# Performance work log

Measured on AMD Instinct MI355X. Metric: run time of the kernel, lower is better.

Reference implementation:

```python
import jax, jax.numpy as jnp
import numpy as np

B = 1024   # env batch (rollout step, T=1)
F = 512    # feature_size ('big' conv tower)
H = 128    # LSTM hidden size


def _conv(x, W, b, stride):
    # x: [B,Cin,H,W], W: [Cout,Cin,kh,kw]  (PyTorch NCHW / OIHW, VALID padding)
    y = jax.lax.conv_general_dilated(x, W, (stride, stride), 'VALID',
                                     dimension_numbers=('NCHW', 'OIHW', 'NCHW'))
    return y + b[None, :, None, None]


def _tower(x, W1, b1, W2, b2, W3, b3, Wl, bl):
    y = jax.nn.relu(_conv(x, W1, b1, 4))   # [B,32,20,20]
    y = jax.nn.relu(_conv(y, W2, b2, 2))   # [B,64,9,9]
    y = jax.nn.relu(_conv(y, W3, b3, 1))   # [B,64,7,7]
    y = y.reshape(y.shape[0], -1)          # [B,3136]
    return jax.nn.relu(y @ Wl.T + bl)      # [B,512]


def _ln(x, g, b):
    m = jnp.mean(x, -1, keepdims=True)
    v = jnp.var(x, -1, keepdims=True)
    return (x - m) * jax.lax.rsqrt(v + 1e-5) * g + b


def setup_inputs() -> dict:
    key = jax.random.key(0)
    ks = iter(jax.random.split(key, 64))
    rn = lambda shape, s=0.05: jax.random.normal(next(ks), shape, jnp.float32) * s
    inp = {
        'x': jax.random.normal(next(ks), (B, 2, 84, 84), jnp.float32),
        'done': (jax.random.uniform(next(ks), (B,)) < 0.1).astype(jnp.float32),
        'h0': rn((1, B, H), 0.1),
        'c0': rn((1, B, H), 0.1),
        # video tower
        'vW1': rn((32, 1, 8, 8)), 'vb1': jnp.zeros((32,), jnp.float32),
        'vW2': rn((64, 32, 4, 4)), 'vb2': jnp.zeros((64,), jnp.float32),
        'vW3': rn((64, 64, 3, 3)), 'vb3': jnp.zeros((64,), jnp.float32),
        'vWl': rn((F, 64 * 7 * 7)), 'vbl': jnp.zeros((F,), jnp.float32),
        # audio tower
        'aW1': rn((32, 1, 8, 8)), 'ab1': jnp.zeros((32,), jnp.float32),
        'aW2': rn((64, 32, 4, 4)), 'ab2': jnp.zeros((64,), jnp.float32),
        'aW3': rn((64, 64, 3, 3)), 'ab3': jnp.zeros((64,), jnp.float32),
        'aWl': rn((F, 64 * 7 * 7)), 'abl': jnp.zeros((F,), jnp.float32),
        # LayerNorms
        'vln_g': jnp.ones((F,), jnp.float32), 'vln_b': jnp.zeros((F,), jnp.float32),
        'aln_g': jnp.ones((F,), jnp.float32), 'aln_b': jnp.zeros((F,), jnp.float32),
        # CASL attention
        'att_vW': rn((32, F)), 'att_vb': jnp.zeros((32,), jnp.float32),
        'att_aW': rn((32, F)), 'att_ab': jnp.zeros((32,), jnp.float32),
        'att_sW': rn((32, H)), 'att_sb': jnp.zeros((32,), jnp.float32),
        'attW': rn((2, 32)), 'attb': jnp.zeros((2,), jnp.float32),
        # LSTM (PyTorch gate order i,f,g,o)
        'Wih': rn((4 * H, F)), 'Whh': rn((4 * H, H)),
        'bih': jnp.zeros((4 * H,), jnp.float32), 'bhh': jnp.zeros((4 * H,), jnp.float32),
    }
    return inp


def reference(x, done, h0, c0,
              vW1, vb1, vW2, vb2, vW3, vb3, vWl, vbl,
              aW1, ab1, aW2, ab2, aW3, ab3, aWl, abl,
              vln_g, vln_b, aln_g, aln_b,
              att_vW, att_vb, att_aW, att_ab, att_sW, att_sb, attW, attb,
              Wih, Whh, bih, bhh):
    # get_states with T=1 rollout step (batch_size = B)
    vf = _ln(_tower(x[:, 0:1], vW1, vb1, vW2, vb2, vW3, vb3, vWl, vbl), vln_g, vln_b)  # [B,512]
    af = _ln(_tower(x[:, 1:2], aW1, ab1, aW2, ab2, aW3, ab3, aWl, abl), aln_g, aln_b)  # [B,512]
    # attention gating
    act = jnp.tanh(vf @ att_vW.T + att_vb + af @ att_aW.T + att_ab
                   + h0[0] @ att_sW.T + att_sb)                    # [B,32]
    w = jax.nn.softmax(act @ attW.T + attb, axis=-1)               # [B,2]
    fused = w[:, 0:1] * vf + w[:, 1:2] * af                        # [B,512]
    # done-masked LSTM cell (single timestep)
    m = (1.0 - done)[:, None]
    h = m * h0[0]
    c = m * c0[0]
    gates = fused @ Wih.T + bih + h @ Whh.T + bhh                  # [B,512]
    i, f, g, o = jnp.split(gates, 4, axis=-1)
    c_new = jax.nn.sigmoid(f) * c + jax.nn.sigmoid(i) * jnp.tanh(g)
    h_new = jax.nn.sigmoid(o) * jnp.tanh(c_new)                    # [B,128]
    return h_new, c_new, vf, af
```

## Files before the change

### kernel.cpp

```cpp
#include <hip/hip_runtime.h>


typedef unsigned short u16;
typedef unsigned int u32;
typedef __attribute__((ext_vector_type(8))) short bf16x8;
typedef __attribute__((ext_vector_type(4))) float f32x4;

__device__ __forceinline__ float b2f(u16 u) {
    union { u32 i; float f; } v; v.i = ((u32)u) << 16; return v.f;
}
__device__ __forceinline__ u16 f2b(float f) {
    union { float f; u32 i; } v; v.f = f;
    u32 r = v.i + 0x7fffu + ((v.i >> 16) & 1u);
    return (u16)(r >> 16);
}
__device__ __forceinline__ void wave_lds_sync() {
    __builtin_amdgcn_wave_barrier();
    __builtin_amdgcn_s_waitcnt(0xC07F);
    __builtin_amdgcn_wave_barrier();
}

__global__ __launch_bounds__(256) void conv1_mfma(
    const float* __restrict__ x, long boff,
    const u16* __restrict__ Wp,
    const float* __restrict__ bias_v, const float* __restrict__ bias_a,
    u16* __restrict__ outp, int Mtot)
{
    __shared__ __attribute__((aligned(16))) u16 As[4 * 2304];

    const int tid = threadIdx.x;
    const int wave = tid >> 6, lane = tid & 63, quad = lane >> 4, l16 = lane & 15;
    const int t = blockIdx.y;
    const u16* Wpt = Wp + t * 2048;
    const float* bias = t ? bias_a : bias_v;
    u16* outt = outp + (long)t * Mtot * 32;

    const int mbase = blockIdx.x * 128 + wave * 32;
    const int rl = lane >> 1, h = lane & 1;
    int m = mbase + rl; if (m > Mtot - 1) m = Mtot - 1;
    const int bl = m / 400, p = m % 400;
    const int oy = p / 20, ox = p % 20;
    const float* F = x + boff + (long)bl * 14112 + t * 7056
                     + (long)(oy * 4) * 84 + ox * 4;

    {
        u16 tmp[32];
#pragma unroll
        for (int rr = 0; rr < 4; ++rr) {
            const int ky = h * 4 + rr;
            float4 v0 = *(const float4*)(F + ky * 84);
            float4 v1 = *(const float4*)(F + ky * 84 + 4);
            tmp[rr * 8 + 0] = f2b(v0.x); tmp[rr * 8 + 1] = f2b(v0.y);
            tmp[rr * 8 + 2] = f2b(v0.z); tmp[rr * 8 + 3] = f2b(v0.w);
            tmp[rr * 8 + 4] = f2b(v1.x); tmp[rr * 8 + 5] = f2b(v1.y);
            tmp[rr * 8 + 6] = f2b(v1.z); tmp[rr * 8 + 7] = f2b(v1.w);
        }
        u16* dst = As + wave * 2304 + rl * 72 + h * 32;
        const uint4* s = (const uint4*)tmp;
        *(uint4*)(dst)      = s[0];
        *(uint4*)(dst + 8)  = s[1];
        *(uint4*)(dst + 16) = s[2];
        *(uint4*)(dst + 24) = s[3];
    }
    wave_lds_sync();

    const u16* rb = As + wave * 2304;
    f32x4 acc[2][2];
#pragma unroll
    for (int mi = 0; mi < 2; ++mi)
#pragma unroll
        for (int ni = 0; ni < 2; ++ni)
            acc[mi][ni] = (f32x4){0.f, 0.f, 0.f, 0.f};

#pragma unroll
    for (int ks = 0; ks < 2; ++ks) {
        bf16x8 af[2], bf[2];
#pragma unroll
        for (int mi = 0; mi < 2; ++mi)
            af[mi] = *(const bf16x8*)(rb + (mi * 16 + l16) * 72 + ks * 32 + quad * 8);
#pragma unroll
        for (int ni = 0; ni < 2; ++ni)
            bf[ni] = *(const bf16x8*)(Wpt + ((ks * 2 + ni) * 64 + lane) * 8);
#pragma unroll
        for (int mi = 0; mi < 2; ++mi)
#pragma unroll
            for (int ni = 0; ni < 2; ++ni)
                acc[mi][ni] = __builtin_amdgcn_mfma_f32_16x16x32_bf16(
                    af[mi], bf[ni], acc[mi][ni], 0, 0, 0);
    }

#pragma unroll
    for (int mi = 0; mi < 2; ++mi)
#pragma unroll
        for (int ni = 0; ni < 2; ++ni) {
            const int col = ni * 16 + l16;
            const float bv = bias[col];
#pragma unroll
            for (int rr = 0; rr < 4; ++rr) {
                const int row = mbase + mi * 16 + quad * 4 + rr;
                if (row < Mtot)
                    outt[(long)row * 32 + col] = f2b(fmaxf(acc[mi][ni][rr] + bv, 0.f));
            }
        }
}

template<int IC, int IH, int IW, int OC, int KH, int KW, int S, int OH, int OW>
__global__ __launch_bounds__(256) void convW_mfma(
    const u16* __restrict__ in, long inTs,
    const u16* __restrict__ Wp, int WpTs,
    const float* __restrict__ bias_v, const float* __restrict__ bias_a,
    u16* __restrict__ outp, long outTs, int Mtot)
{
    constexpr int OP  = OH * OW;
    constexpr int K   = KH * KW * IC;
    constexpr int NF  = OC / 16;
    constexpr int NCH = K / 64;

    __shared__ __attribute__((aligned(16))) u16 As[4 * 2 * 2304];

    const int tid = threadIdx.x;
    const int wave = tid >> 6, lane = tid & 63, quad = lane >> 4, l16 = lane & 15;
    const int t = blockIdx.y;
    const u16* int_ = in + (long)t * inTs;
    const u16* Wpt = Wp + (long)t * WpTs;
    const float* bias = t ? bias_a : bias_v;
    u16* outt = outp + (long)t * outTs;

    const int mbase = blockIdx.x * 128 + wave * 32;
    const int rl = lane >> 1, h = lane & 1;
    int m = mbase + rl; if (m > Mtot - 1) m = Mtot - 1;
    const int bl = m / OP, p = m % OP;
    const int oy = p / OW, ox = p % OW;
    const u16* abase = int_ + (((long)bl * IH + oy * S) * IW + ox * S) * IC + h * 32;

    u16* wbase = As + wave * 4608 + rl * 72 + h * 32;
    const u16* rbase = As + wave * 4608;

    f32x4 acc[2][NF];
#pragma unroll
    for (int mi = 0; mi < 2; ++mi)
#pragma unroll
        for (int ni = 0; ni < NF; ++ni)
            acc[mi][ni] = (f32x4){0.f, 0.f, 0.f, 0.f};

    uint4 pre0, pre1, pre2, pre3;
    {
        const uint4* s = (const uint4*)abase;
        pre0 = s[0]; pre1 = s[1]; pre2 = s[2]; pre3 = s[3];
    }

#pragma unroll
    for (int c = 0; c < NCH; ++c) {
        {
            u16* dst = wbase + (c & 1) * 2304;
            *(uint4*)(dst)      = pre0;
            *(uint4*)(dst + 8)  = pre1;
            *(uint4*)(dst + 16) = pre2;
            *(uint4*)(dst + 24) = pre3;
        }
        if (c + 1 < NCH) {
            const int k0 = (c + 1) * 64;
            const int pos = k0 / IC;
            const int ky = pos / KW, kx = pos - ky * KW;
            const uint4* s = (const uint4*)(abase + ((long)ky * IW + kx) * IC);
            pre0 = s[0]; pre1 = s[1]; pre2 = s[2]; pre3 = s[3];
        }
        wave_lds_sync();

        const u16* rb = rbase + (c & 1) * 2304;
#pragma unroll
        for (int ks = 0; ks < 2; ++ks) {
            bf16x8 af[2], bf[NF];
#pragma unroll
            for (int mi = 0; mi < 2; ++mi)
                af[mi] = *(const bf16x8*)(rb + (mi * 16 + l16) * 72 + ks * 32 + quad * 8);
#pragma unroll
            for (int ni = 0; ni < NF; ++ni)
                bf[ni] = *(const bf16x8*)(Wpt + (((c * 2 + ks) * NF + ni) * 64 + lane) * 8);
#pragma unroll
            for (int mi = 0; mi < 2; ++mi)
#pragma unroll
                for (int ni = 0; ni < NF; ++ni)
                    acc[mi][ni] = __builtin_amdgcn_mfma_f32_16x16x32_bf16(
                        af[mi], bf[ni], acc[mi][ni], 0, 0, 0);
        }
        __builtin_amdgcn_wave_barrier();
    }

#pragma unroll
    for (int mi = 0; mi < 2; ++mi)
#pragma unroll
        for (int ni = 0; ni < NF; ++ni) {
            const int col = ni * 16 + l16;
            const float bv = bias[col];
#pragma unroll
            for (int rr = 0; rr < 4; ++rr) {
                const int row = mbase + mi * 16 + quad * 4 + rr;
                if (row < Mtot)
                    outt[(long)row * OC + col] = f2b(fmaxf(acc[ni < NF ? mi : mi][ni][rr] + bv, 0.f));
            }
        }
}

#define LDSP 40
__global__ __launch_bounds__(256) void gemm_skp(
    const u16* __restrict__ A, const u16* __restrict__ B0,
    const u16* __restrict__ B1,
    float* __restrict__ Cp, int M, int Mhalf, int N, int K, int Kc)
{
    __shared__ __attribute__((aligned(16))) u16 As[128 * LDSP];
    __shared__ __attribute__((aligned(16))) u16 Bs[128 * LDSP];

    const int tid  = threadIdx.x;
    const int wave = tid >> 6, lane = tid & 63;
    const int quad = lane >> 4, l16 = lane & 15;
    const int m0 = blockIdx.y * 128, n0 = blockIdx.x * 128;
    const u16* B = (m0 < Mhalf) ? B0 : B1;
    const int wm = (wave >> 1) * 64, wn = (wave & 1) * 64;
    const int kfrom = blockIdx.z * Kc;
    int kto = kfrom + Kc; if (kto > K) kto = K;
    float* C = Cp + (long)blockIdx.z * M * N;

    f32x4 acc[4][4];
#pragma unroll
    for (int mi = 0; mi < 4; ++mi)
#pragma unroll
        for (int ni = 0; ni < 4; ++ni)
            acc[mi][ni] = (f32x4){0.f, 0.f, 0.f, 0.f};

    for (int k0 = kfrom; k0 < kto; k0 += 32) {
        __syncthreads();
#pragma unroll
        for (int pass = 0; pass < 2; ++pass) {
            int idx = tid + pass * 256;
            int r = idx >> 2, seg = idx & 3;
            int gr = m0 + r; if (gr > M - 1) gr = M - 1;
            uint4 va = *(const uint4*)(A + (long)gr * K + k0 + seg * 8);
            *(uint4*)(As + r * LDSP + seg * 8) = va;
            uint4 vb = *(const uint4*)(B + (long)(n0 + r) * K + k0 + seg * 8);
            *(uint4*)(Bs + r * LDSP + seg * 8) = vb;
        }
        __syncthreads();

        bf16x8 af[4], bfr[4];
#pragma unroll
        for (int mi = 0; mi < 4; ++mi)
            af[mi] = *(const bf16x8*)(As + (wm + mi * 16 + l16) * LDSP + quad * 8);
#pragma unroll
        for (int ni = 0; ni < 4; ++ni)
            bfr[ni] = *(const bf16x8*)(Bs + (wn + ni * 16 + l16) * LDSP + quad * 8);
#pragma unroll
        for (int mi = 0; mi < 4; ++mi)
#pragma unroll
            for (int ni = 0; ni < 4; ++ni)
                acc[mi][ni] = __builtin_amdgcn_mfma_f32_16x16x32_bf16(
                    af[mi], bfr[ni], acc[mi][ni], 0, 0, 0);
    }

#pragma unroll
    for (int mi = 0; mi < 4; ++mi)
#pragma unroll
        for (int ni = 0; ni < 4; ++ni) {
            int col = n0 + wn + ni * 16 + l16;
#pragma unroll
            for (int rr = 0; rr < 4; ++rr) {
                int row = m0 + wm + mi * 16 + quad * 4 + rr;
                if (row < M) C[(long)row * N + col] = acc[mi][ni][rr];
            }
        }
}

__global__ __launch_bounds__(256) void pack_wl(
    const float* __restrict__ vWl, const float* __restrict__ aWl,
    u16* __restrict__ dst)
{
    __shared__ float row[3136];
    const int bid = blockIdx.x, tid = threadIdx.x;
    const int n = bid & 511;
    const float* src = (bid < 512) ? vWl : aWl;
    for (int i = tid; i < 3136; i += 256)
        row[i] = src[(long)n * 3136 + i];
    __syncthreads();
    u16* d = dst + (long)bid * 3136;
    for (int i = tid; i < 3136; i += 256) {
        int p = i >> 6, oc = i & 63;
        d[i] = f2b(row[oc * 49 + p]);
    }
}

__global__ __launch_bounds__(256) void pack_misc(
    const float* __restrict__ vW1, const float* __restrict__ aW1,
    const float* __restrict__ vW2, const float* __restrict__ aW2,
    const float* __restrict__ vW3, const float* __restrict__ aW3,
    const float* __restrict__ avW, const float* __restrict__ aaW,
    const float* __restrict__ asW,
    const float* __restrict__ Wih, const float* __restrict__ Whh,
    u16* __restrict__ Wp1, u16* __restrict__ Wp2, u16* __restrict__ Wp3,
    u16* __restrict__ WTatt, u16* __restrict__ Bcat)
{
    const int idx = blockIdx.x * 256 + threadIdx.x;
    if (idx < 4096) {
        const float* s = (idx < 2048) ? vW1 : aW1;
        int j0 = idx & 2047;
        int jj = j0 & 7, lane = (j0 >> 3) & 63, rest = j0 >> 9;
        int ni = rest & 1, ks = rest >> 1;
        int oc = ni * 16 + (lane & 15);
        int k  = ks * 32 + (lane >> 4) * 8 + jj;
        Wp1[idx] = f2b(s[oc * 64 + k]);
    } else if (idx < 69632) {
        int i = idx - 4096;
        const float* s = (i < 32768) ? vW2 : aW2;
        int j0 = i & 32767;
        int jj = j0 & 7, lane = (j0 >> 3) & 63, rest = j0 >> 9;
        int ni = rest & 3, rest2 = rest >> 2;
        int ks = rest2 & 1, c = rest2 >> 1;
        int oc = ni * 16 + (lane & 15);
        int k  = c * 64 + ks * 32 + (lane >> 4) * 8 + jj;
        int pos = k >> 5, ic = k & 31;
        int ky = pos >> 2, kx = pos & 3;
        Wp2[i] = f2b(s[((oc * 32 + ic) * 4 + ky) * 4 + kx]);
    } else if (idx < 143360) {
        int i = idx - 69632;
        const float* s = (i < 36864) ? vW3 : aW3;
        int j0 = i % 36864;
        int jj = j0 & 7, lane = (j0 >> 3) & 63, rest = j0 >> 9;
        int ni = rest & 3, rest2 = rest >> 2;
        int ks = rest2 & 1, c = rest2 >> 1;
        int oc = ni * 16 + (lane & 15);
        int k  = c * 64 + ks * 32 + (lane >> 4) * 8 + jj;
        int pos = k >> 6, ic = k & 63;
        int ky = pos / 3, kx = pos % 3;
        Wp3[i] = f2b(s[((oc * 64 + ic) * 3 + ky) * 3 + kx]);
    } else if (idx < 180224) {
        int i = idx - 143360;
        int k = i >> 5, j = i & 31;
        float v = (k < 512) ? avW[(long)j * 512 + k]
                : (k < 1024) ? aaW[(long)j * 512 + (k - 512)]
                : asW[(long)j * 128 + (k - 1024)];
        WTatt[i] = f2b(v);
    } else if (idx < 507904) {
        int i = idx - 180224;
        int n = i / 640, k = i % 640;
        Bcat[i] = f2b((k < 512) ? Wih[(long)n * 512 + k]
                                : Whh[(long)n * 128 + (k - 512)]);
    }
}

__global__ __launch_bounds__(256) void ln_attn(
    const float* __restrict__ ychp,
    const float* __restrict__ bl_v, const float* __restrict__ bl_a,
    const float* __restrict__ g_v,  const float* __restrict__ g_a,
    const float* __restrict__ be_v, const float* __restrict__ be_a,
    const float* __restrict__ h0,   const float* __restrict__ done,
    const u16* __restrict__ WT,
    const float* __restrict__ avb, const float* __restrict__ aab,
    const float* __restrict__ asb,
    const float* __restrict__ attW, const float* __restrict__ attb,
    float* __restrict__ vf_out, float* __restrict__ af_out,
    u16* __restrict__ Acat)
{
    __shared__ float vs[512], afs[512], hs[128], red[256], part[8][32], act[32], wsm[2];
    __shared__ float mean_s, inv_s;
    const int b = blockIdx.x, tid = threadIdx.x;

    if (tid < 128) hs[tid] = h0[b * 128 + tid];

#pragma unroll
    for (int tw = 0; tw < 2; ++tw) {
        const long row = tw ? (1024 + b) : b;
        const float* bias = tw ? bl_a : bl_v;
        const float* g    = tw ? g_a  : g_v;
        const float* be   = tw ? be_a : be_v;
        float* fo   = tw ? af_out : vf_out;
        float* dst  = tw ? afs : vs;

        float s0 = bias[tid], s1 = bias[tid + 256];
#pragma unroll
        for (int z = 0; z < 7; ++z) {
            const float* yr = ychp + (long)z * 1048576 + row * 512;
            s0 += yr[tid];
            s1 += yr[tid + 256];
        }
        float v0 = fmaxf(s0, 0.f), v1 = fmaxf(s1, 0.f);

        __syncthreads();
        red[tid] = v0 + v1;
        __syncthreads();
        for (int s = 128; s > 0; s >>= 1) { if (tid < s) red[tid] += red[tid + s]; __syncthreads(); }
        if (tid == 0) mean_s = red[0] * (1.f / 512.f);
        __syncthreads();
        float mean = mean_s;
        float d0 = v0 - mean, d1 = v1 - mean;
        red[tid] = d0 * d0 + d1 * d1;
        __syncthreads();
        for (int s = 128; s > 0; s >>= 1) { if (tid < s) red[tid] += red[tid + s]; __syncthreads(); }
        if (tid == 0) inv_s = rsqrtf(red[0] * (1.f / 512.f) + 1e-5f);
        __syncthreads();
        float inv = inv_s;

        float o0 = d0 * inv * g[tid]       + be[tid];
        float o1 = d1 * inv * g[tid + 256] + be[tid + 256];
        dst[tid] = o0; dst[tid + 256] = o1;
        fo[(long)b * 512 + tid]       = o0;
        fo[(long)b * 512 + tid + 256] = o1;
    }
    __syncthreads();

    {
        const int j = tid & 31, g = tid >> 5;
        float a = 0.f;
#pragma unroll 8
        for (int k = g * 64; k < g * 64 + 64; ++k)
            a += vs[k] * b2f(WT[k * 32 + j]);
#pragma unroll 8
        for (int k = g * 64; k < g * 64 + 64; ++k)
            a += afs[k] * b2f(WT[(512 + k) * 32 + j]);
#pragma unroll 8
        for (int k = g * 16; k < g * 16 + 16; ++k)
            a += hs[k] * b2f(WT[(1024 + k) * 32 + j]);
        part[g][j] = a;
    }
    __syncthreads();
    if (tid < 32) {
        float a = avb[tid] + aab[tid] + asb[tid];
#pragma unroll
        for (int g2 = 0; g2 < 8; ++g2) a += part[g2][tid];
        act[tid] = tanhf(a);
    }
    __syncthreads();
    if (tid == 0) {
        float l0 = attb[0], l1 = attb[1];
        for (int j = 0; j < 32; ++j) {
            l0 += act[j] * attW[j];
            l1 += act[j] * attW[32 + j];
        }
        float mx = fmaxf(l0, l1);
        float e0 = expf(l0 - mx), e1 = expf(l1 - mx);
        float s = e0 + e1;
        wsm[0] = e0 / s; wsm[1] = e1 / s;
    }
    __syncthreads();
    const float w0 = wsm[0], w1 = wsm[1];
    const float m = 1.f - done[b];
    for (int i = tid; i < 512; i += 256)
        Acat[(long)b * 640 + i] = f2b(w0 * vs[i] + w1 * afs[i]);
    if (tid < 128)
        Acat[(long)b * 640 + 512 + tid] = f2b(m * hs[tid]);
}

__global__ __launch_bounds__(128) void lstm_fin(
    const float* __restrict__ gatesp,
    const float* __restrict__ bih, const float* __restrict__ bhh,
    const float* __restrict__ c0, const float* __restrict__ done,
    float* __restrict__ out)
{
    const int b = blockIdx.x, j = threadIdx.x;
    float gi = bih[j]       + bhh[j];
    float gf = bih[128 + j] + bhh[128 + j];
    float gg = bih[256 + j] + bhh[256 + j];
    float go = bih[384 + j] + bhh[384 + j];
#pragma unroll
    for (int z = 0; z < 4; ++z) {
        const float* G = gatesp + (long)z * 524288 + (long)b * 512;
        gi += G[j]; gf += G[128 + j]; gg += G[256 + j]; go += G[384 + j];
    }
    float m  = 1.f - done[b];
    float c  = m * c0[b * 128 + j];
    float si = 1.f / (1.f + expf(-gi));
    float sf = 1.f / (1.f + expf(-gf));
    float so = 1.f / (1.f + expf(-go));
    float cn = sf * c + si * tanhf(gg);
    float hn = so * tanhf(cn);
    out[b * 128 + j]          = hn;
    out[131072 + b * 128 + j] = cn;
}

extern "C" void kernel_launch(void* const* d_in, const int* in_sizes, int n_in,
                              void* d_out, int out_size, void* d_ws, size_t ws_size,
                              hipStream_t stream)
{
    (void)in_sizes; (void)n_in; (void)out_size;

    const float* x     = (const float*)d_in[0];
    const float* done  = (const float*)d_in[1];
    const float* h0    = (const float*)d_in[2];
    const float* c0in  = (const float*)d_in[3];
    const float* vW1   = (const float*)d_in[4];
    const float* vb1   = (const float*)d_in[5];
    const float* vW2   = (const float*)d_in[6];
    const float* vb2   = (const float*)d_in[7];
    const float* vW3   = (const float*)d_in[8];
    const float* vb3   = (const float*)d_in[9];
    const float* vWl   = (const float*)d_in[10];
    const float* vbl   = (const float*)d_in[11];
    const float* aW1   = (const float*)d_in[12];
    const float* ab1   = (const float*)d_in[13];
    const float* aW2   = (const float*)d_in[14];
    const float* ab2   = (const float*)d_in[15];
    const float* aW3   = (const float*)d_in[16];
    const float* ab3   = (const float*)d_in[17];
    const float* aWl   = (const float*)d_in[18];
    const float* abl   = (const float*)d_in[19];
    const float* vln_g = (const float*)d_in[20];
    const float* vln_b = (const float*)d_in[21];
    const float* aln_g = (const float*)d_in[22];
    const float* aln_b = (const float*)d_in[23];
    const float* att_vW = (const float*)d_in[24];
    const float* att_vb = (const float*)d_in[25];
    const float* att_aW = (const float*)d_in[26];
    const float* att_ab = (const float*)d_in[27];
    const float* att_sW = (const float*)d_in[28];
    const float* att_sb = (const float*)d_in[29];
    const float* attW  = (const float*)d_in[30];
    const float* attb  = (const float*)d_in[31];
    const float* Wih   = (const float*)d_in[32];
    const float* Whh   = (const float*)d_in[33];
    const float* bih   = (const float*)d_in[34];
    const float* bhh   = (const float*)d_in[35];

    float* out = (float*)d_out;
    float* vf_out = out + 262144;
    float* af_out = out + 786432;

    const size_t PERBATCH = 2ul * (12800 + 5184) * 2;
    const size_t PERSIST  =
          4ul * 1024 * 512 * 4
        + 7ul * 2048 * 512 * 4
        + 1024ul * 640 * 2
        + 512ul * 640 * 2
        + 2ul * 512 * 3136 * 2
        + 2ul * 2048 * 2
        + 2ul * 32768 * 2
        + 2ul * 36864 * 2
        + 36864ul * 2
        + 2ul * 1024 * 3136 * 2;
    int NB = 64;
    const int cands[4] = {1024, 512, 256, 128};
    for (int i = 0; i < 4; ++i)
        if (PERSIST + (size_t)cands[i] * PERBATCH <= ws_size) { NB = cands[i]; break; }
    const int NC = 1024 / NB;

    char* p = (char*)d_ws;
    float* gatesp = (float*)p; p += 4ul * 1024 * 512 * 4;
    float* ychp   = (float*)p; p += 7ul * 2048 * 512 * 4;
    u16*   Acat   = (u16*)p;   p += 1024ul * 640 * 2;
    u16*   Bcat   = (u16*)p;   p += 512ul * 640 * 2;
    u16*   Wlb    = (u16*)p;   p += 2ul * 512 * 3136 * 2;
    u16*   Wp1    = (u16*)p;   p += 2ul * 2048 * 2;
    u16*   Wp2    = (u16*)p;   p += 2ul * 32768 * 2;
    u16*   Wp3    = (u16*)p;   p += 2ul * 36864 * 2;
    u16*   WTatt  = (u16*)p;   p += 36864ul * 2;
    u16*   c3f    = (u16*)p;   p += 2ul * 1024 * 3136 * 2;
    u16*   c1     = (u16*)p;   p += 2ul * NB * 12800 * 2;
    u16*   c2     = (u16*)p;

    hipLaunchKernelGGL(pack_wl, dim3(1024), dim3(256), 0, stream, vWl, aWl, Wlb);
    hipLaunchKernelGGL(pack_misc, dim3(1984), dim3(256), 0, stream,
        vW1, aW1, vW2, aW2, vW3, aW3, att_vW, att_aW, att_sW, Wih, Whh,
        Wp1, Wp2, Wp3, WTatt, Bcat);

    for (int cch = 0; cch < NC; ++cch) {
        const int b0 = cch * NB;
        const int M1 = NB * 400, M2 = NB * 81, M3 = NB * 49;

        hipLaunchKernelGGL(conv1_mfma, dim3(M1 / 128, 2), dim3(256), 0, stream,
            x, (long)b0 * 14112, Wp1, vb1, ab1, c1, M1);

        hipLaunchKernelGGL((convW_mfma<32, 20, 20, 64, 4, 4, 2, 9, 9>),
            dim3((M2 + 127) / 128, 2), dim3(256), 0, stream,
            c1, (long)NB * 12800, Wp2, 32768, vb2, ab2,
            c2, (long)NB * 5184, M2);

        hipLaunchKernelGGL((convW_mfma<64, 9, 9, 64, 3, 3, 1, 7, 7>),
            dim3((M3 + 127) / 128, 2), dim3(256), 0, stream,
            c2, (long)NB * 5184, Wp3, 36864, vb3, ab3,
            c3f + (long)b0 * 3136, 1024l * 3136, M3);
    }

    hipLaunchKernelGGL(gemm_skp, dim3(4, 16, 7), dim3(256), 0, stream,
        c3f, Wlb, Wlb + 512ul * 3136, ychp, 2048, 1024, 512, 3136, 448);

    hipLaunchKernelGGL(ln_attn, dim3(1024), dim3(256), 0, stream,
        ychp, vbl, abl, vln_g, aln_g, vln_b, aln_b, h0, done, WTatt,
        att_vb, att_ab, att_sb, attW, attb, vf_out, af_out, Acat);

    hipLaunchKernelGGL(gemm_skp, dim3(4, 8, 4), dim3(256), 0, stream,
        Acat, Bcat, Bcat, gatesp, 1024, 1 << 30, 512, 640, 160);

    hipLaunchKernelGGL(lstm_fin, dim3(1024), dim3(128), 0, stream,
        gatesp, bih, bhh, c0in, done, out);
}
```

Measured before the change: 297.5 us.

## Load conv A-fragments directly from global, widen M tiles, fuse packing, shuffle LayerNorm

The conv kernels no longer stage the im2col tile through LDS. Each lane now loads its MFMA A-fragment straight from global memory, and each wave covers 64 output rows instead of 32, which halves the grid and doubles the accumulators. The two weight-packing kernels are merged into one launch. The LayerNorm reduction now uses wave shuffles and computes variance in a single pass as E[x^2]-mean^2, instead of two tree reductions in LDS. These changes cut LDS traffic, barriers and launch count, at the cost of more register pressure, less coalesced global loads and slightly different numerics for the variance.

```diff
diff --git a/kernel.cpp b/kernel.cpp
--- a/kernel.cpp
+++ b/kernel.cpp
@@ -13,11 +13,6 @@
     union { float f; u32 i; } v; v.f = f;
     u32 r = v.i + 0x7fffu + ((v.i >> 16) & 1u);
     return (u16)(r >> 16);
-}
-__device__ __forceinline__ void wave_lds_sync() {
-    __builtin_amdgcn_wave_barrier();
-    __builtin_amdgcn_s_waitcnt(0xC07F);
-    __builtin_amdgcn_wave_barrier();
 }
 
 __global__ __launch_bounds__(256) void conv1_mfma(
@@ -26,8 +21,6 @@
     const float* __restrict__ bias_v, const float* __restrict__ bias_a,
     u16* __restrict__ outp, int Mtot)
 {
-    __shared__ __attribute__((aligned(16))) u16 As[4 * 2304];
-
     const int tid = threadIdx.x;
     const int wave = tid >> 6, lane = tid & 63, quad = lane >> 4, l16 = lane & 15;
     const int t = blockIdx.y;
@@ -35,62 +28,50 @@
     const float* bias = t ? bias_a : bias_v;
     u16* outt = outp + (long)t * Mtot * 32;
 
-    const int mbase = blockIdx.x * 128 + wave * 32;
-    const int rl = lane >> 1, h = lane & 1;
-    int m = mbase + rl; if (m > Mtot - 1) m = Mtot - 1;
-    const int bl = m / 400, p = m % 400;
-    const int oy = p / 20, ox = p % 20;
-    const float* F = x + boff + (long)bl * 14112 + t * 7056
-                     + (long)(oy * 4) * 84 + ox * 4;
-
-    {
-        u16 tmp[32];
-#pragma unroll
-        for (int rr = 0; rr < 4; ++rr) {
-            const int ky = h * 4 + rr;
-            float4 v0 = *(const float4*)(F + ky * 84);
-            float4 v1 = *(const float4*)(F + ky * 84 + 4);
-            tmp[rr * 8 + 0] = f2b(v0.x); tmp[rr * 8 + 1] = f2b(v0.y);
-            tmp[rr * 8 + 2] = f2b(v0.z); tmp[rr * 8 + 3] = f2b(v0.w);
-            tmp[rr * 8 + 4] = f2b(v1.x); tmp[rr * 8 + 5] = f2b(v1.y);
-            tmp[rr * 8 + 6] = f2b(v1.z); tmp[rr * 8 + 7] = f2b(v1.w);
-        }
-        u16* dst = As + wave * 2304 + rl * 72 + h * 32;
-        const uint4* s = (const uint4*)tmp;
-        *(uint4*)(dst)      = s[0];
-        *(uint4*)(dst + 8)  = s[1];
-        *(uint4*)(dst + 16) = s[2];
-        *(uint4*)(dst + 24) = s[3];
-    }
-    wave_lds_sync();
-
-    const u16* rb = As + wave * 2304;
-    f32x4 acc[2][2];
-#pragma unroll
-    for (int mi = 0; mi < 2; ++mi)
+    const int mbase = blockIdx.x * 256 + wave * 64;
+
+    const float* Fm[4];
+#pragma unroll
+    for (int mi = 0; mi < 4; ++mi) {
+        int m = mbase + mi * 16 + l16; if (m > Mtot - 1) m = Mtot - 1;
+        const int bl = m / 400, p = m % 400;
+        const int oy = p / 20, ox = p % 20;
+        Fm[mi] = x + boff + (long)bl * 14112 + t * 7056
+               + (long)(oy * 4) * 84 + ox * 4;
+    }
+
+    f32x4 acc[4][2];
+#pragma unroll
+    for (int mi = 0; mi < 4; ++mi)
 #pragma unroll
         for (int ni = 0; ni < 2; ++ni)
             acc[mi][ni] = (f32x4){0.f, 0.f, 0.f, 0.f};
 
 #pragma unroll
     for (int ks = 0; ks < 2; ++ks) {
-        bf16x8 af[2], bf[2];
-#pragma unroll
-        for (int mi = 0; mi < 2; ++mi)
-            af[mi] = *(const bf16x8*)(rb + (mi * 16 + l16) * 72 + ks * 32 + quad * 8);
+        bf16x8 bfr[2];
 #pragma unroll
         for (int ni = 0; ni < 2; ++ni)
-            bf[ni] = *(const bf16x8*)(Wpt + ((ks * 2 + ni) * 64 + lane) * 8);
-#pragma unroll
-        for (int mi = 0; mi < 2; ++mi)
+            bfr[ni] = *(const bf16x8*)(Wpt + ((ks * 2 + ni) * 64 + lane) * 8);
+#pragma unroll
+        for (int mi = 0; mi < 4; ++mi) {
+            const float* Fp = Fm[mi] + (ks * 4 + quad) * 84;
+            float4 v0 = *(const float4*)(Fp);
+            float4 v1 = *(const float4*)(Fp + 4);
+            bf16x8 a;
+            a[0] = (short)f2b(v0.x); a[1] = (short)f2b(v0.y);
+            a[2] = (short)f2b(v0.z); a[3] = (short)f2b(v0.w);
+            a[4] = (short)f2b(v1.x); a[5] = (short)f2b(v1.y);
+            a[6] = (short)f2b(v1.z); a[7] = (short)f2b(v1.w);
 #pragma unroll
             for (int ni = 0; ni < 2; ++ni)
                 acc[mi][ni] = __builtin_amdgcn_mfma_f32_16x16x32_bf16(
-                    af[mi], bf[ni], acc[mi][ni], 0, 0, 0);
-    }
-
-#pragma unroll
-    for (int mi = 0; mi < 2; ++mi)
+                    a, bfr[ni], acc[mi][ni], 0, 0, 0);
+        }
+    }
+
+#pragma unroll
+    for (int mi = 0; mi < 4; ++mi)
 #pragma unroll
         for (int ni = 0; ni < 2; ++ni) {
             const int col = ni * 16 + l16;
@@ -115,8 +96,6 @@
     constexpr int K   = KH * KW * IC;
     constexpr int NF  = OC / 16;
     constexpr int NCH = K / 64;
-
-    __shared__ __attribute__((aligned(16))) u16 As[4 * 2 * 2304];
 
     const int tid = threadIdx.x;
     const int wave = tid >> 6, lane = tid & 63, quad = lane >> 4, l16 = lane & 15;
@@ -126,69 +105,50 @@
     const float* bias = t ? bias_a : bias_v;
     u16* outt = outp + (long)t * outTs;
 
-    const int mbase = blockIdx.x * 128 + wave * 32;
-    const int rl = lane >> 1, h = lane & 1;
-    int m = mbase + rl; if (m > Mtot - 1) m = Mtot - 1;
-    const int bl = m / OP, p = m % OP;
-    const int oy = p / OW, ox = p % OW;
-    const u16* abase = int_ + (((long)bl * IH + oy * S) * IW + ox * S) * IC + h * 32;
-
-    u16* wbase = As + wave * 4608 + rl * 72 + h * 32;
-    const u16* rbase = As + wave * 4608;
-
-    f32x4 acc[2][NF];
-#pragma unroll
-    for (int mi = 0; mi < 2; ++mi)
+    const int mbase = blockIdx.x * 256 + wave * 64;
+
+    const u16* Am[4];
+#pragma unroll
+    for (int mi = 0; mi < 4; ++mi) {
+        int m = mbase + mi * 16 + l16; if (m > Mtot - 1) m = Mtot - 1;
+        const int bl = m / OP, p = m % OP;
+        const int oy = p / OW, ox = p % OW;
+        Am[mi] = int_ + (((long)bl * IH + oy * S) * IW + ox * S) * IC + quad * 8;
+    }
+
+    f32x4 acc[4][NF];
+#pragma unroll
+    for (int mi = 0; mi < 4; ++mi)
 #pragma unroll
         for (int ni = 0; ni < NF; ++ni)
             acc[mi][ni] = (f32x4){0.f, 0.f, 0.f, 0.f};
 
-    uint4 pre0, pre1, pre2, pre3;
-    {
-        const uint4* s = (const uint4*)abase;
-        pre0 = s[0]; pre1 = s[1]; pre2 = s[2]; pre3 = s[3];
-    }
-
 #pragma unroll
     for (int c = 0; c < NCH; ++c) {
-        {
-            u16* dst = wbase + (c & 1) * 2304;
-            *(uint4*)(dst)      = pre0;
-            *(uint4*)(dst + 8)  = pre1;
-            *(uint4*)(dst + 16) = pre2;
-            *(uint4*)(dst + 24) = pre3;
-        }
-        if (c + 1 < NCH) {
-            const int k0 = (c + 1) * 64;
-            const int pos = k0 / IC;
-            const int ky = pos / KW, kx = pos - ky * KW;
-            const uint4* s = (const uint4*)(abase + ((long)ky * IW + kx) * IC);
-            pre0 = s[0]; pre1 = s[1]; pre2 = s[2]; pre3 = s[3];
-        }
-        wave_lds_sync();
-
-        const u16* rb = rbase + (c & 1) * 2304;
 #pragma unroll
         for (int ks = 0; ks < 2; ++ks) {
-            bf16x8 af[2], bf[NF];
-#pragma unroll
-            for (int mi = 0; mi < 2; ++mi)
-                af[mi] = *(const bf16x8*)(rb + (mi * 16 + l16) * 72 + ks * 32 + quad * 8);
+            const int koff = c * 64 + ks * 32;
+            const int pos = koff / IC, ic0 = koff % IC;
+            const int ky = pos / KW, kx = pos % KW;
+            const int off = (ky * IW + kx) * IC + ic0;
+            bf16x8 af[4], bfr[NF];
+#pragma unroll
+            for (int mi = 0; mi < 4; ++mi)
+                af[mi] = *(const bf16x8*)(Am[mi] + off);
 #pragma unroll
             for (int ni = 0; ni < NF; ++ni)
-                bf[ni] = *(const bf16x8*)(Wpt + (((c * 2 + ks) * NF + ni) * 64 + lane) * 8);
-#pragma unroll
-            for (int mi = 0; mi < 2; ++mi)
+                bfr[ni] = *(const bf16x8*)(Wpt + (((c * 2 + ks) * NF + ni) * 64 + lane) * 8);
+#pragma unroll
+            for (int mi = 0; mi < 4; ++mi)
 #pragma unroll
                 for (int ni = 0; ni < NF; ++ni)
                     acc[mi][ni] = __builtin_amdgcn_mfma_f32_16x16x32_bf16(
-                        af[mi], bf[ni], acc[mi][ni], 0, 0, 0);
-        }
-        __builtin_amdgcn_wave_barrier();
-    }
-
-#pragma unroll
-    for (int mi = 0; mi < 2; ++mi)
+                        af[mi], bfr[ni], acc[mi][ni], 0, 0, 0);
+        }
+    }
+
+#pragma unroll
+    for (int mi = 0; mi < 4; ++mi)
 #pragma unroll
         for (int ni = 0; ni < NF; ++ni) {
             const int col = ni * 16 + l16;
@@ -197,7 +157,7 @@
             for (int rr = 0; rr < 4; ++rr) {
                 const int row = mbase + mi * 16 + quad * 4 + rr;
                 if (row < Mtot)
-                    outt[(long)row * OC + col] = f2b(fmaxf(acc[ni < NF ? mi : mi][ni][rr] + bv, 0.f));
+                    outt[(long)row * OC + col] = f2b(fmaxf(acc[mi][ni][rr] + bv, 0.f));
             }
         }
 }
@@ -270,35 +230,36 @@
         }
 }
 
-__global__ __launch_bounds__(256) void pack_wl(
+__global__ __launch_bounds__(256) void pack_all(
     const float* __restrict__ vWl, const float* __restrict__ aWl,
-    u16* __restrict__ dst)
-{
-    __shared__ float row[3136];
-    const int bid = blockIdx.x, tid = threadIdx.x;
-    const int n = bid & 511;
-    const float* src = (bid < 512) ? vWl : aWl;
-    for (int i = tid; i < 3136; i += 256)
-        row[i] = src[(long)n * 3136 + i];
-    __syncthreads();
-    u16* d = dst + (long)bid * 3136;
-    for (int i = tid; i < 3136; i += 256) {
-        int p = i >> 6, oc = i & 63;
-        d[i] = f2b(row[oc * 49 + p]);
-    }
-}
-
-__global__ __launch_bounds__(256) void pack_misc(
     const float* __restrict__ vW1, const float* __restrict__ aW1,
     const float* __restrict__ vW2, const float* __restrict__ aW2,
     const float* __restrict__ vW3, const float* __restrict__ aW3,
     const float* __restrict__ avW, const float* __restrict__ aaW,
     const float* __restrict__ asW,
     const float* __restrict__ Wih, const float* __restrict__ Whh,
+    u16* __restrict__ Wlb,
     u16* __restrict__ Wp1, u16* __restrict__ Wp2, u16* __restrict__ Wp3,
     u16* __restrict__ WTatt, u16* __restrict__ Bcat)
 {
-    const int idx = blockIdx.x * 256 + threadIdx.x;
+    __shared__ float row[3136];
+    const int bid = blockIdx.x, tid = threadIdx.x;
+
+    if (bid < 1024) {
+        const int n = bid & 511;
+        const float* src = (bid < 512) ? vWl : aWl;
+        for (int i = tid; i < 3136; i += 256)
+            row[i] = src[(long)n * 3136 + i];
+        __syncthreads();
+        u16* d = Wlb + (long)bid * 3136;
+        for (int i = tid; i < 3136; i += 256) {
+            int p = i >> 6, oc = i & 63;
+            d[i] = f2b(row[oc * 49 + p]);
+        }
+        return;
+    }
+
+    const int idx = (bid - 1024) * 256 + tid;
     if (idx < 4096) {
         const float* s = (idx < 2048) ? vW1 : aW1;
         int j0 = idx & 2047;
@@ -359,9 +320,10 @@
     float* __restrict__ vf_out, float* __restrict__ af_out,
     u16* __restrict__ Acat)
 {
-    __shared__ float vs[512], afs[512], hs[128], red[256], part[8][32], act[32], wsm[2];
-    __shared__ float mean_s, inv_s;
+    __shared__ float vs[512], afs[512], hs[128], part[8][32], act[32], wsm[2];
+    __shared__ float redS[4], redQ[4];
     const int b = blockIdx.x, tid = threadIdx.x;
+    const int lane = tid & 63, wv = tid >> 6;
 
     if (tid < 128) hs[tid] = h0[b * 128 + tid];
 
@@ -383,28 +345,27 @@
         }
         float v0 = fmaxf(s0, 0.f), v1 = fmaxf(s1, 0.f);
 
+        float sum = v0 + v1, sq = v0 * v0 + v1 * v1;
+#pragma unroll
+        for (int o = 32; o; o >>= 1) {
+            sum += __shfl_xor(sum, o);
+            sq  += __shfl_xor(sq, o);
+        }
+        if (lane == 0) { redS[wv] = sum; redQ[wv] = sq; }
         __syncthreads();
-        red[tid] = v0 + v1;
-        __syncthreads();
-        for (int s = 128; s > 0; s >>= 1) { if (tid < s) red[tid] += red[tid + s]; __syncthreads(); }
-        if (tid == 0) mean_s = red[0] * (1.f / 512.f);
-        __syncthreads();
-        float mean = mean_s;
-        float d0 = v0 - mean, d1 = v1 - mean;
-        red[tid] = d0 * d0 + d1 * d1;
-        __syncthreads();
-        for (int s = 128; s > 0; s >>= 1) { if (tid < s) red[tid] += red[tid + s]; __syncthreads(); }
-        if (tid == 0) inv_s = rsqrtf(red[0] * (1.f / 512.f) + 1e-5f);
-        __syncthreads();
-        float inv = inv_s;
-
-        float o0 = d0 * inv * g[tid]       + be[tid];
-        float o1 = d1 * inv * g[tid + 256] + be[tid + 256];
+        const float ts = redS[0] + redS[1] + redS[2] + redS[3];
+        const float tq = redQ[0] + redQ[1] + redQ[2] + redQ[3];
+        const float mean = ts * (1.f / 512.f);
+        const float var  = tq * (1.f / 512.f) - mean * mean;
+        const float inv  = rsqrtf(var + 1e-5f);
+
+        float o0 = (v0 - mean) * inv * g[tid]       + be[tid];
+        float o1 = (v1 - mean) * inv * g[tid + 256] + be[tid + 256];
         dst[tid] = o0; dst[tid + 256] = o1;
         fo[(long)b * 512 + tid]       = o0;
         fo[(long)b * 512 + tid + 256] = o1;
-    }
-    __syncthreads();
+        __syncthreads();
+    }
 
     {
         const int j = tid & 31, g = tid >> 5;
@@ -554,25 +515,24 @@
     u16*   c1     = (u16*)p;   p += 2ul * NB * 12800 * 2;
     u16*   c2     = (u16*)p;
 
-    hipLaunchKernelGGL(pack_wl, dim3(1024), dim3(256), 0, stream, vWl, aWl, Wlb);
-    hipLaunchKernelGGL(pack_misc, dim3(1984), dim3(256), 0, stream,
-        vW1, aW1, vW2, aW2, vW3, aW3, att_vW, att_aW, att_sW, Wih, Whh,
-        Wp1, Wp2, Wp3, WTatt, Bcat);
+    hipLaunchKernelGGL(pack_all, dim3(3008), dim3(256), 0, stream,
+        vWl, aWl, vW1, aW1, vW2, aW2, vW3, aW3, att_vW, att_aW, att_sW,
+        Wih, Whh, Wlb, Wp1, Wp2, Wp3, WTatt, Bcat);
 
     for (int cch = 0; cch < NC; ++cch) {
         const int b0 = cch * NB;
         const int M1 = NB * 400, M2 = NB * 81, M3 = NB * 49;
 
-        hipLaunchKernelGGL(conv1_mfma, dim3(M1 / 128, 2), dim3(256), 0, stream,
+        hipLaunchKernelGGL(conv1_mfma, dim3((M1 + 255) / 256, 2), dim3(256), 0, stream,
             x, (long)b0 * 14112, Wp1, vb1, ab1, c1, M1);
 
         hipLaunchKernelGGL((convW_mfma<32, 20, 20, 64, 4, 4, 2, 9, 9>),
-            dim3((M2 + 127) / 128, 2), dim3(256), 0, stream,
+            dim3((M2 + 255) / 256, 2), dim3(256), 0, stream,
             c1, (long)NB * 12800, Wp2, 32768, vb2, ab2,
             c2, (long)NB * 5184, M2);
 
         hipLaunchKernelGGL((convW_mfma<64, 9, 9, 64, 3, 3, 1, 7, 7>),
-            dim3((M3 + 127) / 128, 2), dim3(256), 0, stream,
+            dim3((M3 + 255) / 256, 2), dim3(256), 0, stream,
             c2, (long)NB * 5184, Wp3, 36864, vb3, ab3,
             c3f + (long)b0 * 3136, 1024l * 3136, M3);
     }
```

New measurement: 312.2 us. +4.9%, slower.
